# Performance work log

Hardware: AMD Instinct MI355X
Metric: run time of the kernel (lower is better)

## Reference

```python
import jax, jax.numpy as jnp
import numpy as np

VOCAB_P1 = 100001  # vocab_size + 1
EMB_DIM = 128
BATCH = 256
NNZ_Q = 2048
NNZ_D = 262144


def setup_inputs() -> dict:
    key = jax.random.key(0)
    ks = jax.random.split(key, 10)
    return {
        "q_rows": jax.random.randint(ks[0], (NNZ_Q,), 0, VOCAB_P1, dtype=jnp.int32),
        "q_cols": jax.random.randint(ks[1], (NNZ_Q,), 0, BATCH, dtype=jnp.int32),
        "q_vals": jax.random.uniform(ks[2], (NNZ_Q,), dtype=jnp.float32),
        "d_rows": jax.random.randint(ks[3], (NNZ_D,), 0, VOCAB_P1, dtype=jnp.int32),
        "d_cols": jax.random.randint(ks[4], (NNZ_D,), 0, BATCH, dtype=jnp.int32),
        "d_freqs": jax.random.uniform(ks[5], (NNZ_D,), dtype=jnp.float32),
        "emb": jax.random.normal(ks[6], (VOCAB_P1, EMB_DIM), dtype=jnp.float32) * 0.1,
        "W1": jax.random.normal(ks[7], (EMB_DIM, 100), dtype=jnp.float32) * (2.0 / EMB_DIM) ** 0.5,
        "b1": jnp.zeros((100,), dtype=jnp.float32),
        "W2": jax.random.normal(ks[8], (100, 1), dtype=jnp.float32) * (2.0 / 100) ** 0.5,
        "b2": jnp.ones((1,), dtype=jnp.float32),
        "mu": jnp.float32(2500.0),
        "batch_size": BATCH,
    }


def _scatter_dense(rows, cols, vals, batch_size):
    # tf.sparse.to_dense: dense [vocab+1, batch] with values at (row, col).
    # Indices are (assumed) unique, so add == set; add keeps it a clean scatter.
    return jnp.zeros((VOCAB_P1, batch_size), vals.dtype).at[rows, cols].add(vals)


def reference(q_rows, q_cols, q_vals, d_rows, d_cols, d_freqs,
              emb, W1, b1, W2, b2, mu, batch_size):
    # query bag-of-words dense tensor [V, B]
    q = _scatter_dense(q_rows, q_cols, q_vals, batch_size)

    # term discrimination value MLP on document terms (dropout disabled = eval mode)
    h = jax.nn.relu(emb[d_rows] @ W1 + b1)          # [nnz_d, 100]
    tdv = jax.nn.relu(h @ W2 + b2)[:, 0]            # [nnz_d]
    freq_tdv = tdv * d_freqs                        # [nnz_d]

    # weighted document term-frequency dense tensor [V, B]
    d = _scatter_dense(d_rows, d_cols, freq_tdv, batch_size)

    cfreq = jnp.sum(d, axis=1) / jnp.sum(d)                     # [V]
    smoothing = jnp.log(mu / (jnp.sum(d, axis=0) + mu))         # [B]
    dir_d = jnp.log1p(d / (1.0 + mu * cfreq[:, None])) + smoothing  # [V, B]
    rel = jnp.sum(q * dir_d, axis=0)                            # [B]
    return (rel, d)
```

## Files before the change

kernel.cpp:

```cpp
#include <hip/hip_runtime.h>
#include <stdint.h>

#define VOCAB_P1 100001
#define EMB_DIM  128
#define BATCH    256
#define NNZ_Q    2048
#define NNZ_D    262144

#define NPAD 112
#define ROWP 136
#define NGRP 6251

#define WS_ZERO_FLOATS (100352 + 256)

typedef __attribute__((ext_vector_type(8))) short  short8;
typedef __attribute__((ext_vector_type(4))) float  float4v;

__device__ __forceinline__ unsigned short f2bf(float f) {
    union { float f; unsigned u; } v; v.f = f;
    unsigned u = v.u;
    u += 0x7fffu + ((u >> 16) & 1u);
    return (unsigned short)(u >> 16);
}

__device__ __forceinline__ short8 cvt8(float4 a, float4 b) {
    short8 r;
    r[0] = (short)f2bf(a.x); r[1] = (short)f2bf(a.y);
    r[2] = (short)f2bf(a.z); r[3] = (short)f2bf(a.w);
    r[4] = (short)f2bf(b.x); r[5] = (short)f2bf(b.y);
    r[6] = (short)f2bf(b.z); r[7] = (short)f2bf(b.w);
    return r;
}

__global__ __launch_bounds__(256) void zero_kernel(
    float4* __restrict__ a, int n4a, float4* __restrict__ b, int n4b)
{
    const float4 z = {0.f, 0.f, 0.f, 0.f};
    int stride = gridDim.x * 256;
    for (int i = blockIdx.x * 256 + threadIdx.x; i < n4a; i += stride)
        a[i] = z;
    for (int i = blockIdx.x * 256 + threadIdx.x; i < n4b; i += stride)
        b[i] = z;
}

__global__ __launch_bounds__(256) void mlp_tdv_kernel(
    const float* __restrict__ emb, const float* __restrict__ W1,
    const float* __restrict__ b1, const float* __restrict__ W2,
    const float* __restrict__ b2, float* __restrict__ tdvtab)
{
    __shared__ __align__(16) short w1t[NPAD * ROWP];
    __shared__ float b1s[NPAD];
    __shared__ float w2s[NPAD];

    const int tid = threadIdx.x;

    int* w1i = (int*)w1t;
    for (int i = tid; i < NPAD * ROWP / 2; i += 256) w1i[i] = 0;
    __syncthreads();
    for (int f = tid; f < EMB_DIM * 100; f += 256) {
        int k = f / 100, j = f - k * 100;
        w1t[j * ROWP + k] = (short)f2bf(W1[f]);
    }
    if (tid < NPAD) {
        b1s[tid] = (tid < 100) ? b1[tid] : 0.f;
        w2s[tid] = (tid < 100) ? W2[tid] : 0.f;
    }
    __syncthreads();

    const int lane = tid & 63;
    const int w    = tid >> 6;
    const int col  = lane & 15;
    const int quad = lane >> 4;
    const float b2v = b2[0];
    const int nw = gridDim.x * 4;

    for (int grp = blockIdx.x * 4 + w; grp < NGRP; grp += nw) {
        int r  = grp * 16 + col;
        int rr = (r <= VOCAB_P1 - 1) ? r : (VOCAB_P1 - 1);
        const float* rp = emb + (size_t)rr * EMB_DIM + quad * 8;
        float4 u0 = *(const float4*)(rp);
        float4 u1 = *(const float4*)(rp + 4);
        float4 u2 = *(const float4*)(rp + 32);
        float4 u3 = *(const float4*)(rp + 36);
        float4 u4 = *(const float4*)(rp + 64);
        float4 u5 = *(const float4*)(rp + 68);
        float4 u6 = *(const float4*)(rp + 96);
        float4 u7 = *(const float4*)(rp + 100);
        short8 a0 = cvt8(u0, u1), a1 = cvt8(u2, u3);
        short8 a2 = cvt8(u4, u5), a3 = cvt8(u6, u7);

        float s0 = 0.f, s1 = 0.f, s2 = 0.f, s3 = 0.f;
        for (int jt = 0; jt < 7; ++jt) {
            const short* bp = &w1t[(jt * 16 + col) * ROWP + quad * 8];
            short8 bv0 = *(const short8*)(bp);
            short8 bv1 = *(const short8*)(bp + 32);
            short8 bv2 = *(const short8*)(bp + 64);
            short8 bv3 = *(const short8*)(bp + 96);

            float4v acc = {0.f, 0.f, 0.f, 0.f};
            acc = __builtin_amdgcn_mfma_f32_16x16x32_bf16(a0, bv0, acc, 0, 0, 0);
            acc = __builtin_amdgcn_mfma_f32_16x16x32_bf16(a1, bv1, acc, 0, 0, 0);
            acc = __builtin_amdgcn_mfma_f32_16x16x32_bf16(a2, bv2, acc, 0, 0, 0);
            acc = __builtin_amdgcn_mfma_f32_16x16x32_bf16(a3, bv3, acc, 0, 0, 0);

            float b1v = b1s[jt * 16 + col];
            float w2v = w2s[jt * 16 + col];
            float h;
            h = acc[0] + b1v; h = h > 0.f ? h : 0.f; s0 += h * w2v;
            h = acc[1] + b1v; h = h > 0.f ? h : 0.f; s1 += h * w2v;
            h = acc[2] + b1v; h = h > 0.f ? h : 0.f; s2 += h * w2v;
            h = acc[3] + b1v; h = h > 0.f ? h : 0.f; s3 += h * w2v;
        }
        for (int m = 1; m < 16; m <<= 1) {
            s0 += __shfl_xor(s0, m, 64);
            s1 += __shfl_xor(s1, m, 64);
            s2 += __shfl_xor(s2, m, 64);
            s3 += __shfl_xor(s3, m, 64);
        }
        if (col < 4) {
            float sv = (col == 0) ? s0 : (col == 1) ? s1 : (col == 2) ? s2 : s3;
            int row = grp * 16 + quad * 4 + col;
            if (row < VOCAB_P1) {
                float tdv = sv + b2v;
                tdvtab[row] = tdv > 0.f ? tdv : 0.f;
            }
        }
    }
}

__global__ __launch_bounds__(256) void scatter_kernel(
    const int* __restrict__ d_rows, const int* __restrict__ d_cols,
    const float* __restrict__ d_freqs, const float* __restrict__ tdvtab,
    float* __restrict__ dmat, float* __restrict__ rowsum,
    float* __restrict__ colsum)
{
    __shared__ float cs[BATCH];
    const int tid = threadIdx.x;
    cs[tid] = 0.f;
    __syncthreads();

    int e = blockIdx.x * 256 + tid;
    int   r = d_rows[e];
    int   c = d_cols[e];
    float f = d_freqs[e];
    float ft = tdvtab[r] * f;

    atomicAdd(&dmat[(size_t)r * BATCH + c], ft);
    atomicAdd(&rowsum[r], ft);
    atomicAdd(&cs[c], ft);

    __syncthreads();
    atomicAdd(&colsum[tid], cs[tid]);
}

__global__ __launch_bounds__(256) void rel_kernel(
    const int* __restrict__ q_rows, const int* __restrict__ q_cols,
    const float* __restrict__ q_vals, const float* __restrict__ dmat,
    const float* __restrict__ rowsum, const float* __restrict__ colsum,
    const float* __restrict__ mu_p, float* __restrict__ rel)
{
    __shared__ float csh[BATCH];
    __shared__ float red[BATCH];
    const int tid = threadIdx.x;
    float c = colsum[tid];
    csh[tid] = c;
    red[tid] = c;
    __syncthreads();
    for (int s = 128; s > 0; s >>= 1) {
        if (tid < s) red[tid] += red[tid + s];
        __syncthreads();
    }
    float tot = red[0];
    float mu  = mu_p[0];

    int e = blockIdx.x * 256 + tid;
    int v = q_rows[e], b = q_cols[e];
    float dval = dmat[(size_t)v * BATCH + b];
    float cf   = rowsum[v] / tot;
    float dir  = log1pf(dval / (1.f + mu * cf)) + logf(mu / (csh[b] + mu));
    atomicAdd(&rel[b], q_vals[e] * dir);
}

extern "C" void kernel_launch(void* const* d_in, const int* in_sizes, int n_in,
                              void* d_out, int out_size, void* d_ws, size_t ws_size,
                              hipStream_t stream)
{
    const int*   q_rows  = (const int*)d_in[0];
    const int*   q_cols  = (const int*)d_in[1];
    const float* q_vals  = (const float*)d_in[2];
    const int*   d_rows  = (const int*)d_in[3];
    const int*   d_cols  = (const int*)d_in[4];
    const float* d_freqs = (const float*)d_in[5];
    const float* emb     = (const float*)d_in[6];
    const float* W1      = (const float*)d_in[7];
    const float* b1      = (const float*)d_in[8];
    const float* W2      = (const float*)d_in[9];
    const float* b2      = (const float*)d_in[10];
    const float* mu      = (const float*)d_in[11];

    float* rel  = (float*)d_out;
    float* dmat = rel + BATCH;

    float* rowsum = (float*)d_ws;
    float* colsum = rowsum + 100352;
    float* tdvtab = colsum + 256;

    zero_kernel<<<2048, 256, 0, stream>>>(
        (float4*)d_out, out_size / 4, (float4*)d_ws, WS_ZERO_FLOATS / 4);

    mlp_tdv_kernel<<<1024, 256, 0, stream>>>(emb, W1, b1, W2, b2, tdvtab);
    scatter_kernel<<<NNZ_D / 256, 256, 0, stream>>>(
        d_rows, d_cols, d_freqs, tdvtab, dmat, rowsum, colsum);
    rel_kernel<<<NNZ_Q / 256, 256, 0, stream>>>(
        q_rows, q_cols, q_vals, dmat, rowsum, colsum, mu, rel);
}
```

Baseline: 240.9 us.

## Fuse zeroing into MLP launch, drop rowsum atomics, compute row sums in rel

Result: faster. 204.8 us (-15.0%).

```diff
diff --git a/kernel.cpp b/kernel.cpp
--- a/kernel.cpp
+++ b/kernel.cpp
@@ -10,8 +10,9 @@
 #define NPAD 112
 #define ROWP 136
 #define NGRP 6251
-
-#define WS_ZERO_FLOATS (100352 + 256)
+#define ZBLK 256
+#define MBLK 1024
+#define OUT_F4 6400128
 
 typedef __attribute__((ext_vector_type(8))) short  short8;
 typedef __attribute__((ext_vector_type(4))) float  float4v;
@@ -32,27 +33,26 @@
     return r;
 }
 
-__global__ __launch_bounds__(256) void zero_kernel(
-    float4* __restrict__ a, int n4a, float4* __restrict__ b, int n4b)
-{
-    const float4 z = {0.f, 0.f, 0.f, 0.f};
-    int stride = gridDim.x * 256;
-    for (int i = blockIdx.x * 256 + threadIdx.x; i < n4a; i += stride)
-        a[i] = z;
-    for (int i = blockIdx.x * 256 + threadIdx.x; i < n4b; i += stride)
-        b[i] = z;
-}
-
-__global__ __launch_bounds__(256) void mlp_tdv_kernel(
+__global__ __launch_bounds__(256) void zero_mlp_kernel(
+    float* __restrict__ d_out_f, float* __restrict__ colsum2,
     const float* __restrict__ emb, const float* __restrict__ W1,
     const float* __restrict__ b1, const float* __restrict__ W2,
     const float* __restrict__ b2, float* __restrict__ tdvtab)
 {
+    const int tid = threadIdx.x;
+
+    if (blockIdx.x < ZBLK) {
+        const float4 z = {0.f, 0.f, 0.f, 0.f};
+        float4* dst = (float4*)d_out_f;
+        int i0 = blockIdx.x * 256 + tid;
+        for (int i = i0; i < OUT_F4; i += ZBLK * 256) dst[i] = z;
+        if (i0 < 128) ((float4*)colsum2)[i0] = z;
+        return;
+    }
+
     __shared__ __align__(16) short w1t[NPAD * ROWP];
     __shared__ float b1s[NPAD];
     __shared__ float w2s[NPAD];
-
-    const int tid = threadIdx.x;
 
     int* w1i = (int*)w1t;
     for (int i = tid; i < NPAD * ROWP / 2; i += 256) w1i[i] = 0;
@@ -72,9 +72,9 @@
     const int col  = lane & 15;
     const int quad = lane >> 4;
     const float b2v = b2[0];
-    const int nw = gridDim.x * 4;
-
-    for (int grp = blockIdx.x * 4 + w; grp < NGRP; grp += nw) {
+    const int bid  = blockIdx.x - ZBLK;
+
+    for (int grp = bid * 4 + w; grp < NGRP; grp += MBLK * 4) {
         int r  = grp * 16 + col;
         int rr = (r <= VOCAB_P1 - 1) ? r : (VOCAB_P1 - 1);
         const float* rp = emb + (size_t)rr * EMB_DIM + quad * 8;
@@ -131,54 +131,61 @@
 __global__ __launch_bounds__(256) void scatter_kernel(
     const int* __restrict__ d_rows, const int* __restrict__ d_cols,
     const float* __restrict__ d_freqs, const float* __restrict__ tdvtab,
-    float* __restrict__ dmat, float* __restrict__ rowsum,
-    float* __restrict__ colsum)
+    float* __restrict__ dmat, float* __restrict__ colsum2)
 {
     __shared__ float cs[BATCH];
     const int tid = threadIdx.x;
     cs[tid] = 0.f;
     __syncthreads();
 
-    int e = blockIdx.x * 256 + tid;
-    int   r = d_rows[e];
-    int   c = d_cols[e];
-    float f = d_freqs[e];
-    float ft = tdvtab[r] * f;
-
-    atomicAdd(&dmat[(size_t)r * BATCH + c], ft);
-    atomicAdd(&rowsum[r], ft);
-    atomicAdd(&cs[c], ft);
-
-    __syncthreads();
-    atomicAdd(&colsum[tid], cs[tid]);
+    int g = blockIdx.x * 256 + tid;
+    int2   r2 = ((const int2*)d_rows)[g];
+    int2   c2 = ((const int2*)d_cols)[g];
+    float2 f2 = ((const float2*)d_freqs)[g];
+
+    float ft0 = tdvtab[r2.x] * f2.x;
+    float ft1 = tdvtab[r2.y] * f2.y;
+
+    atomicAdd(&dmat[(size_t)r2.x * BATCH + c2.x], ft0);
+    atomicAdd(&dmat[(size_t)r2.y * BATCH + c2.y], ft1);
+    atomicAdd(&cs[c2.x], ft0);
+    atomicAdd(&cs[c2.y], ft1);
+
+    __syncthreads();
+    atomicAdd(&colsum2[(blockIdx.x & 1) * BATCH + tid], cs[tid]);
 }
 
 __global__ __launch_bounds__(256) void rel_kernel(
     const int* __restrict__ q_rows, const int* __restrict__ q_cols,
     const float* __restrict__ q_vals, const float* __restrict__ dmat,
-    const float* __restrict__ rowsum, const float* __restrict__ colsum,
-    const float* __restrict__ mu_p, float* __restrict__ rel)
-{
-    __shared__ float csh[BATCH];
-    __shared__ float red[BATCH];
-    const int tid = threadIdx.x;
-    float c = colsum[tid];
-    csh[tid] = c;
-    red[tid] = c;
-    __syncthreads();
-    for (int s = 128; s > 0; s >>= 1) {
-        if (tid < s) red[tid] += red[tid + s];
-        __syncthreads();
-    }
-    float tot = red[0];
-    float mu  = mu_p[0];
-
-    int e = blockIdx.x * 256 + tid;
+    const float* __restrict__ colsum2, const float* __restrict__ mu_p,
+    float* __restrict__ rel)
+{
+    const int tid  = threadIdx.x;
+    const int lane = tid & 63;
+    const int e    = blockIdx.x * 4 + (tid >> 6);
+
     int v = q_rows[e], b = q_cols[e];
-    float dval = dmat[(size_t)v * BATCH + b];
-    float cf   = rowsum[v] / tot;
-    float dir  = log1pf(dval / (1.f + mu * cf)) + logf(mu / (csh[b] + mu));
-    atomicAdd(&rel[b], q_vals[e] * dir);
+    float qv = q_vals[e];
+    float mu = mu_p[0];
+
+    float4 cv  = *(const float4*)(colsum2 + lane * 4);
+    float4 cv2 = *(const float4*)(colsum2 + BATCH + lane * 4);
+    float4 rv  = *(const float4*)(dmat + (size_t)v * BATCH + lane * 4);
+    float tot_p = cv.x + cv.y + cv.z + cv.w + cv2.x + cv2.y + cv2.z + cv2.w;
+    float row_p = rv.x + rv.y + rv.z + rv.w;
+    for (int m = 1; m < 64; m <<= 1) {
+        tot_p += __shfl_xor(tot_p, m, 64);
+        row_p += __shfl_xor(row_p, m, 64);
+    }
+
+    if (lane == 0) {
+        float csb  = colsum2[b] + colsum2[BATCH + b];
+        float dval = dmat[(size_t)v * BATCH + b];
+        float cf   = row_p / tot_p;
+        float dir  = log1pf(dval / (1.f + mu * cf)) + logf(mu / (csb + mu));
+        atomicAdd(&rel[b], qv * dir);
+    }
 }
 
 extern "C" void kernel_launch(void* const* d_in, const int* in_sizes, int n_in,
@@ -201,16 +208,13 @@
     float* rel  = (float*)d_out;
     float* dmat = rel + BATCH;
 
-    float* rowsum = (float*)d_ws;
-    float* colsum = rowsum + 100352;
-    float* tdvtab = colsum + 256;
-
-    zero_kernel<<<2048, 256, 0, stream>>>(
-        (float4*)d_out, out_size / 4, (float4*)d_ws, WS_ZERO_FLOATS / 4);
-
-    mlp_tdv_kernel<<<1024, 256, 0, stream>>>(emb, W1, b1, W2, b2, tdvtab);
-    scatter_kernel<<<NNZ_D / 256, 256, 0, stream>>>(
-        d_rows, d_cols, d_freqs, tdvtab, dmat, rowsum, colsum);
-    rel_kernel<<<NNZ_Q / 256, 256, 0, stream>>>(
-        q_rows, q_cols, q_vals, dmat, rowsum, colsum, mu, rel);
-}
+    float* colsum2 = (float*)d_ws;
+    float* tdvtab  = colsum2 + 2 * BATCH;
+
+    zero_mlp_kernel<<<ZBLK + MBLK, 256, 0, stream>>>(
+        (float*)d_out, colsum2, emb, W1, b1, W2, b2, tdvtab);
+    scatter_kernel<<<NNZ_D / 512, 256, 0, stream>>>(
+        d_rows, d_cols, d_freqs, tdvtab, dmat, colsum2);
+    rel_kernel<<<NNZ_Q / 4, 256, 0, stream>>>(
+        q_rows, q_cols, q_vals, dmat, colsum2, mu, rel);
+}
```
